# Kernel tuning notes

Hardware: AMD Instinct MI355X
Metric: run time of the kernel (lower is better)

Reference implementation:

```python
import jax, jax.numpy as jnp
import numpy as np
from functools import lru_cache


@lru_cache(maxsize=None)
def _mw_basis(L):
    """Fully-normalized associated Legendre basis on MW-style theta grid.

    Returns (Pfull, w):
      Pfull: (L, 2L-1, L) float32, Pfull[l, L-1+m, t] = Nbar_lm * P_l^m(cos theta_t)
             (zero for |m| > l), with Y_lm = Pfull * exp(i m phi).
      w:     (L,) float32 quadrature weights sin(theta)*dtheta*dphi.
    """
    t = np.arange(L)
    theta = np.pi * (2 * t + 1) / (2 * L - 1)  # MW theta samples
    ct, st = np.cos(theta), np.sin(theta)
    P = np.zeros((L, L, L))
    P[0, 0] = np.full(L, np.sqrt(1.0 / (4.0 * np.pi)))
    for m in range(1, L):
        P[m, m] = -np.sqrt((2.0 * m + 1.0) / (2.0 * m)) * st * P[m - 1, m - 1]
    for m in range(L - 1):
        P[m + 1, m] = np.sqrt(2.0 * m + 3.0) * ct * P[m, m]
    for m in range(L):
        for l in range(m + 2, L):
            a = np.sqrt((4.0 * l * l - 1.0) / (l * l - m * m))
            b = np.sqrt(((2.0 * l + 1.0) * (l - 1 - m) * (l - 1 + m)) / ((2.0 * l - 3.0) * (l * l - m * m)))
            P[l, m] = a * ct * P[l - 1, m] - b * P[l - 2, m]
    Pfull = np.zeros((L, 2 * L - 1, L), dtype=np.float32)
    for m in range(L):
        Pfull[:, L - 1 + m, :] = P[:, m, :]
        if m > 0:
            Pfull[:, L - 1 - m, :] = ((-1.0) ** m) * P[:, m, :]
    dang = 2.0 * np.pi / (2 * L - 1)  # theta and phi spacing
    w = (st * dang * dang).astype(np.float32)
    return jnp.asarray(Pfull), jnp.asarray(w)


def sht_forward(x):
    """x: (L, 2L-1, C) real -> flm: (L, 2L-1, C) complex, m indexed -(L-1)..(L-1)."""
    L = x.shape[0]
    P, w = _mw_basis(L)
    F = jnp.fft.fft(x.astype(jnp.complex64), axis=1)           # k = 0..2L-2
    F = jnp.concatenate([F[:, L:, :], F[:, :L, :]], axis=1)     # reorder to m = -(L-1)..L-1
    # flm = sum_t w_t Nbar P_l^m(theta_t) * Fm(theta_t)
    return jnp.einsum('lmt,tmc->lmc', P * w[None, None, :], F)


def sht_inverse(flm):
    """flm: (L, 2L-1, C) complex -> f: (L, 2L-1, C) complex on MW grid."""
    L = flm.shape[0]
    P, _ = _mw_basis(L)
    G = jnp.einsum('lmc,lmt->tmc', flm, P)                      # (theta, m, C)
    G = jnp.concatenate([G[:, L - 1:, :], G[:, :L - 1, :]], axis=1)  # m order -> fft k order
    return jnp.fft.ifft(G, axis=1) * (2 * L - 1)


def zero_pad_flm(flm, L_out):
    L_in = flm.shape[0]
    p = L_out - L_in
    return jnp.pad(flm, ((0, p), (p, p), (0, 0)))


L_IN = 256
L_FREQ = 128
L_OUT = 256
C_IN = 32
C_OUT = 32
T_DIM = 256


def setup_inputs() -> dict:
    key = jax.random.key(0)
    ks = jax.random.split(key, 8)
    return {
        'x': jax.random.normal(ks[0], (L_IN, 2 * L_IN - 1, C_IN), jnp.float32),
        't_emb': jax.random.normal(ks[1], (T_DIM,), jnp.float32),
        'weight_real': 0.02 * jax.random.normal(ks[2], (L_FREQ, C_IN, C_OUT), jnp.float32),
        'weight_imag': 0.02 * jax.random.normal(ks[3], (L_FREQ, C_IN, C_OUT), jnp.float32),
        'w_tr': jax.random.normal(ks[4], (T_DIM, L_FREQ), jnp.float32) / np.sqrt(T_DIM),
        'b_tr': jnp.zeros((L_FREQ,), jnp.float32),
        'w_ti': jax.random.normal(ks[5], (T_DIM, L_FREQ), jnp.float32) / np.sqrt(T_DIM),
        'b_ti': jnp.zeros((L_FREQ,), jnp.float32),
    }


def reference(x, t_emb, weight_real, weight_imag, w_tr, b_tr, w_ti, b_ti):
    # forward SHT over all channels at once
    flm = sht_forward(x)                                       # (L_in, 2L_in-1, C_in) complex64
    # bilinear resize of the spectrum to the used bandlimit (real/imag separately)
    tgt = (L_FREQ, 2 * L_FREQ - 1, flm.shape[2])
    flm = (jax.image.resize(jnp.real(flm), tgt, 'bilinear')
           + 1j * jax.image.resize(jnp.imag(flm), tgt, 'bilinear'))
    # time-modulated per-degree complex spectral weights
    t_cplx = (t_emb @ w_tr + b_tr) + 1j * (t_emb @ w_ti + b_ti)   # (L_freq,)
    weight = t_cplx[:, None, None] * (weight_real + 1j * weight_imag)  # (L_freq, C_in, C_out)
    flm = jnp.einsum('lmi,lio->lmo', flm, weight)
    # zero pad to output bandlimit and inverse SHT
    flm = zero_pad_flm(flm, L_OUT)                             # (L_out, 2L_out-1, C_out)
    x_out = jnp.real(sht_inverse(flm))
    return x_out
```

## Files before the change

### kernel.cpp

```cpp
#include <hip/hip_runtime.h>
#include <math.h>

#define PI_D 3.14159265358979323846

typedef short v8s __attribute__((ext_vector_type(8)));
typedef float v4f __attribute__((ext_vector_type(4)));

constexpr size_t OFF_PA   = 0;
constexpr size_t OFF_PT   = 8388608;
constexpr size_t OFF_SFRE = 12582912;
constexpr size_t OFF_SFIM = 14680064;
constexpr size_t OFF_FRE  = 16777216;
constexpr size_t OFF_FIM  = 18874368;
constexpr size_t OFF_CRE  = 20971520;
constexpr size_t OFF_CIM  = 22016000;
constexpr size_t OFF_AF   = 23060480;
constexpr size_t OFF_AI   = 23191552;
constexpr size_t OFF_WQ   = 23322624;
constexpr size_t OFF_TC   = 23322880;
constexpr size_t OFF_WLW  = 23323136;
constexpr size_t OFF_WLI  = 23323648;
constexpr size_t OFF_WMW  = 23324160;
constexpr size_t OFF_WMI  = 23325696;
constexpr size_t OFF_GRE  = OFF_FRE;
constexpr size_t OFF_GIM  = OFF_FIM;

__device__ __forceinline__ short f2bf(float f) {
  unsigned u = __float_as_uint(f);
  unsigned r = (u + 0x7FFFu + ((u >> 16) & 1u)) >> 16;
  return (short)r;
}

__global__ void k_prep(const float* t_emb, const float* w_tr, const float* b_tr,
                       const float* w_ti, const float* b_ti, float* ws) {
  int bx = blockIdx.x, tid = threadIdx.x;
  if (bx < 2048) {
    int g = bx * 256 + tid;
    bool inv = (g >= 262144);
    int gid = inv ? g - 262144 : g;
    int j = gid & 7, lane = (gid >> 3) & 63, ks = (gid >> 9) & 15, mt = gid >> 13;
    int m = mt * 16 + (lane & 15);
    int k = ks * 32 + ((lane >> 4) << 3) + j;
    float v = 0.f;
    if (!inv) {
      if (k < 511) {
        int mm = (m < 256) ? m : m - 256;
        int kk = (mm * k) % 511;
        float ang = (float)(2.0 * PI_D / 511.0) * (float)kk;
        float s, c; __sincosf(ang, &s, &c);
        v = (m < 256) ? c : -s;
      }
      ((short*)(ws + OFF_AF))[gid] = f2bf(v);
    } else {
      if (m < 511 && k < 510) {
        int jj = (k < 255) ? k : k - 255;
        int jm = jj - 127;
        int kk = ((jm * m) % 511 + 511) % 511;
        float ang = (float)(2.0 * PI_D / 511.0) * (float)kk;
        float s, c; __sincosf(ang, &s, &c);
        v = (k < 255) ? c : -s;
      }
      ((short*)(ws + OFF_AI))[gid] = f2bf(v);
    }
    return;
  }
  if (tid < 256) {
    double theta = PI_D * (2.0 * tid + 1.0) / 511.0;
    double dang = 2.0 * PI_D / 511.0;
    ws[OFF_WQ + tid] = (float)(sin(theta) * dang * dang);
  }
  {
    int h = tid >> 7, o = tid & 127;
    const float* W = h ? w_ti : w_tr;
    float s = h ? b_ti[o] : b_tr[o];
    for (int T = 0; T < 256; ++T) s += t_emb[T] * W[T * 128 + o];
    ws[OFF_TC + h * 128 + o] = s;
  }
  if (tid < 128) {
    double sf = 2.0 * tid + 0.5;
    double wv[4]; int iv[4]; double wsum = 0.0;
    for (int a = 0; a < 4; ++a) {
      int t = 2 * tid - 1 + a;
      double r = 1.0 - fabs(sf - (double)t) * 0.5;
      bool valid = (t >= 0 && t < 256 && r > 0.0);
      wv[a] = valid ? r : 0.0; iv[a] = valid ? t : 0;
      wsum += wv[a];
    }
    for (int a = 0; a < 4; ++a) {
      ws[OFF_WLW + tid * 4 + a] = (float)(wv[a] / wsum);
      ((int*)(ws + OFF_WLI))[tid * 4 + a] = iv[a];
    }
  }
  if (tid < 255) {
    double inv2 = 511.0 / 255.0;
    double sf = (tid + 0.5) * inv2 - 0.5;
    int t0 = (int)floor(sf) - 2;
    double wv[6]; int iv[6]; double wsum = 0.0;
    for (int b = 0; b < 6; ++b) {
      int t = t0 + b;
      double r = 1.0 - fabs(sf - (double)t) * (255.0 / 511.0);
      bool valid = (t >= 0 && t < 511 && r > 0.0);
      wv[b] = valid ? r : 0.0; iv[b] = valid ? t : 0;
      wsum += wv[b];
    }
    for (int b = 0; b < 6; ++b) {
      ws[OFF_WMW + tid * 6 + b] = (float)(wv[b] / wsum);
      ((int*)(ws + OFF_WMI))[tid * 6 + b] = iv[b];
    }
  }
}

__global__ __launch_bounds__(256) void k_legendre(float* ws) {
  int m = blockIdx.x, t = threadIdx.x;
  __shared__ double cA[256], cB[256], cS[256];
  {
    int l = t;
    if (l >= 1) cS[l] = -sqrt((2.0 * l + 1.0) / (2.0 * l));
    if (l >= m + 2) {
      double ll = l, mm = m;
      double den = ll * ll - mm * mm;
      cA[l] = sqrt((4.0 * ll * ll - 1.0) / den);
      cB[l] = sqrt((2.0 * ll + 1.0) * (ll - 1.0 - mm) * (ll - 1.0 + mm) /
                   ((2.0 * ll - 3.0) * den));
    }
  }
  __syncthreads();
  __shared__ short tile[16 * 280];
  __shared__ short tileT[256 * 34];
  bool wantPT = (m < 128);
  short* PAp = (short*)(ws + OFF_PA) + (size_t)m * 65536;
  short* PTp = (short*)(ws + OFF_PT) + (size_t)m * 65536;
  double theta = PI_D * (2.0 * t + 1.0) / 511.0;
  double ct = cos(theta), st = sin(theta);
  double p0 = sqrt(1.0 / (4.0 * PI_D));
  for (int k = 1; k <= m; ++k) p0 *= cS[k] * st;
  double pm1 = 0.0, pcur = 0.0;
  for (int lt = 0; lt < 16; ++lt) {
    for (int li = 0; li < 16; ++li) {
      int l = lt * 16 + li;
      float v;
      if (l < m) v = 0.f;
      else if (l == m) { pcur = p0; v = (float)pcur; }
      else if (l == m + 1) { pm1 = pcur; pcur = sqrt(2.0 * m + 3.0) * ct * pm1; v = (float)pcur; }
      else { double p2 = cA[l] * ct * pcur - cB[l] * pm1; pm1 = pcur; pcur = p2; v = (float)p2; }
      short bv = f2bf(v);
      tile[li * 280 + t] = bv;
      if (wantPT) tileT[t * 34 + li] = bv;
    }
    __syncthreads();
#pragma unroll
    for (int pass = 0; pass < 2; ++pass) {
      int ch = pass * 256 + t;
      int li = ch & 15, T0 = ch >> 4;
      size_t dst = (size_t)lt * 4096 + (size_t)(T0 >> 2) * 512 + (size_t)((T0 & 3) * 16 + li) * 8;
      *(v8s*)(PAp + dst) = *(const v8s*)(tile + li * 280 + T0 * 8);
    }
    if (wantPT) {
#pragma unroll
      for (int pass = 0; pass < 2; ++pass) {
        int ch = pass * 256 + t;
        int tt = ch >> 1, li0 = (ch & 1) * 8;
        size_t dst = (size_t)(tt >> 4) * 4096 + (size_t)(lt >> 1) * 512 +
                     (size_t)(((lt & 1) * 2 + (li0 >> 3)) * 16 + (tt & 15)) * 8;
        const int* src = (const int*)(tileT + tt * 34 + li0);
        int* d = (int*)(PTp + dst);
        d[0] = src[0]; d[1] = src[1]; d[2] = src[2]; d[3] = src[3];
      }
    }
    __syncthreads();
  }
}

__global__ __launch_bounds__(256) void k_gemm_f(const float* x, float* ws) {
  int bx = blockIdx.x, t = blockIdx.y;
  int nt = bx & 1, mh = bx >> 1;
  int tid = threadIdx.x, wave = tid >> 6, lane = tid & 63;
  const v8s* A = (const v8s*)(ws + OFF_AF);
  float wq = ws[OFF_WQ + t];
  const float* xb = x + (size_t)t * 511 * 32 + nt * 16 + (lane & 15);
  int phiB = (lane >> 4) << 3;
  int mtB = mh * 16 + wave * 4;
  v4f acc[4];
#pragma unroll
  for (int i = 0; i < 4; ++i) acc[i] = (v4f){0.f, 0.f, 0.f, 0.f};
  float bv[8];
#pragma unroll
  for (int j = 0; j < 8; ++j) {
    int phi = phiB + j;
    bv[j] = (phi < 511) ? xb[(size_t)phi * 32] : 0.f;
  }
  for (int ks = 0; ks < 16; ++ks) {
    float bn[8];
    if (ks < 15) {
      int phi0 = (ks + 1) * 32 + phiB;
#pragma unroll
      for (int j = 0; j < 8; ++j) {
        int phi = phi0 + j;
        bn[j] = (phi < 511) ? xb[(size_t)phi * 32] : 0.f;
      }
    }
    v8s b;
#pragma unroll
    for (int j = 0; j < 8; ++j) b[j] = f2bf(wq * bv[j]);
#pragma unroll
    for (int i = 0; i < 4; ++i) {
      v8s a = A[(size_t)((mtB + i) * 16 + ks) * 64 + lane];
      acc[i] = __builtin_amdgcn_mfma_f32_16x16x32_bf16(a, b, acc[i], 0, 0, 0);
    }
    if (ks < 15) {
#pragma unroll
      for (int j = 0; j < 8; ++j) bv[j] = bn[j];
    }
  }
  int quad = lane >> 4, cn = nt * 16 + (lane & 15);
#pragma unroll
  for (int i = 0; i < 4; ++i) {
    int mt = mtB + i;
#pragma unroll
    for (int r = 0; r < 4; ++r) {
      int mp = mt * 16 + quad * 4 + r;
      float v = acc[i][r];
      if (mp < 256) ws[OFF_FRE + ((size_t)mp * 256 + t) * 32 + cn] = v;
      else          ws[OFF_FIM + ((size_t)(mp - 256) * 256 + t) * 32 + cn] = v;
    }
  }
}

__global__ __launch_bounds__(1024) void k_legfwd(float* ws) {
  int m = blockIdx.x;
  int tid = threadIdx.x, mt = tid >> 6, lane = tid & 63;
  const v8s* A = (const v8s*)(ws + OFF_PA) + (size_t)m * 8192;
  int cl = lane & 15, tB = (lane >> 4) << 3;
  int quad = lane >> 4;
  v4f acc[4];
#pragma unroll
  for (int n = 0; n < 4; ++n) acc[n] = (v4f){0.f, 0.f, 0.f, 0.f};
  bool sk = (mt * 16 + 15) < m;
  if (!sk) {
    const float* Fb[4];
#pragma unroll
    for (int n = 0; n < 4; ++n) {
      int cp = n * 16 + cl;
      Fb[n] = ws + (cp < 32 ? OFF_FRE : OFF_FIM) + (size_t)m * 8192 + (size_t)tB * 32 + (cp & 31);
    }
    float bv[4][8];
#pragma unroll
    for (int n = 0; n < 4; ++n)
#pragma unroll
      for (int j = 0; j < 8; ++j) bv[n][j] = Fb[n][(size_t)j * 32];
    for (int ks = 0; ks < 8; ++ks) {
      float bn[4][8];
      if (ks < 7) {
#pragma unroll
        for (int n = 0; n < 4; ++n)
#pragma unroll
          for (int j = 0; j < 8; ++j) bn[n][j] = Fb[n][(size_t)((ks + 1) * 32 + j) * 32];
      }
      v8s a = A[(size_t)mt * 512 + ks * 64 + lane];
#pragma unroll
      for (int n = 0; n < 4; ++n) {
        v8s b;
#pragma unroll
        for (int j = 0; j < 8; ++j) b[j] = f2bf(bv[n][j]);
        acc[n] = __builtin_amdgcn_mfma_f32_16x16x32_bf16(a, b, acc[n], 0, 0, 0);
      }
      if (ks < 7) {
#pragma unroll
        for (int n = 0; n < 4; ++n)
#pragma unroll
          for (int j = 0; j < 8; ++j) bv[n][j] = bn[n][j];
      }
    }
  }
#pragma unroll
  for (int n = 0; n < 4; ++n) {
    int cp = n * 16 + cl;
    float* dst = ws + ((cp >= 32) ? OFF_SFIM : OFF_SFRE) + (size_t)m * 8192 + (cp & 31);
#pragma unroll
    for (int r = 0; r < 4; ++r) {
      int l = mt * 16 + quad * 4 + r;
      dst[(size_t)l * 32] = sk ? 0.f : acc[n][r];
    }
  }
}

__global__ __launch_bounds__(256) void k_conv(const float* w_real, const float* w_imag, float* ws) {
  int jq = blockIdx.x, l = blockIdx.y;
  int tid = threadIdx.x;
  int jl = tid >> 5, o = tid & 31;
  __shared__ __align__(16) float wr[32 * 36];
  __shared__ __align__(16) float wi[32 * 36];
  __shared__ __align__(16) float fr[8 * 32];
  __shared__ __align__(16) float fi[8 * 32];
  {
    int oo = tid >> 3, i4 = (tid & 7) * 4;
    float tcr = ws[OFF_TC + l], tci = ws[OFF_TC + 128 + l];
#pragma unroll
    for (int q = 0; q < 4; ++q) {
      int i = i4 + q;
      float a = w_real[(size_t)l * 1024 + i * 32 + oo];
      float b = w_imag[(size_t)l * 1024 + i * 32 + oo];
      wr[oo * 36 + i] = tcr * a - tci * b;
      wi[oo * 36 + i] = tcr * b + tci * a;
    }
  }
  const float* SFRE = ws + OFF_SFRE;
  const float* SFIM = ws + OFF_SFIM;
  const float* WMW = ws + OFF_WMW;
  const int* WMI = (const int*)(ws + OFF_WMI);
  float wl[4]; int liv[4];
#pragma unroll
  for (int a = 0; a < 4; ++a) {
    wl[a] = ws[OFF_WLW + l * 4 + a];
    liv[a] = ((const int*)(ws + OFF_WLI))[l * 4 + a];
  }
  for (int ji = 0; ji < 8; ++ji) {
    int j = jq * 64 + ji * 8 + jl;
    int jp = (j < 255) ? j : 254;
    float accr = 0.f, acci = 0.f;
    for (int b = 0; b < 6; ++b) {
      float wm = WMW[jp * 6 + b];
      int jm = WMI[jp * 6 + b];
      bool mneg = (jm < 255);
      int mm = mneg ? (255 - jm) : (jm - 255);
      float fre_f = (mneg && (mm & 1)) ? -1.f : 1.f;
      float fim_f = mneg ? -fre_f : 1.f;
#pragma unroll
      for (int a = 0; a < 4; ++a) {
        float w = wm * wl[a];
        size_t base = ((size_t)mm * 256 + liv[a]) * 32 + o;
        accr = fmaf(w * fre_f, SFRE[base], accr);
        acci = fmaf(w * fim_f, SFIM[base], acci);
      }
    }
    __syncthreads();
    fr[jl * 32 + o] = accr;
    fi[jl * 32 + o] = acci;
    __syncthreads();
    float sr = 0.f, si = 0.f;
#pragma unroll
    for (int i0 = 0; i0 < 32; i0 += 4) {
      float4 f_r = *(const float4*)(fr + jl * 32 + i0);
      float4 f_i = *(const float4*)(fi + jl * 32 + i0);
      float4 w_r = *(const float4*)(wr + o * 36 + i0);
      float4 w_i = *(const float4*)(wi + o * 36 + i0);
      sr += f_r.x * w_r.x - f_i.x * w_i.x;  si += f_r.x * w_i.x + f_i.x * w_r.x;
      sr += f_r.y * w_r.y - f_i.y * w_i.y;  si += f_r.y * w_i.y + f_i.y * w_r.y;
      sr += f_r.z * w_r.z - f_i.z * w_i.z;  si += f_r.z * w_i.z + f_i.z * w_r.z;
      sr += f_r.w * w_r.w - f_i.w * w_i.w;  si += f_r.w * w_i.w + f_i.w * w_r.w;
    }
    if (j < 255) {
      float s = (j < 127 && ((127 - j) & 1)) ? -1.f : 1.f;
      ws[OFF_CRE + ((size_t)j * 128 + l) * 32 + o] = s * sr;
      ws[OFF_CIM + ((size_t)j * 128 + l) * 32 + o] = s * si;
    }
  }
}

__global__ __launch_bounds__(1024) void k_gemm_linv(float* ws) {
  int j = blockIdx.x;
  int d = j - 127; int mm = (d < 0) ? -d : d;
  int tid = threadIdx.x, mt = tid >> 6, lane = tid & 63;
  const v8s* A = (const v8s*)(ws + OFF_PT) + (size_t)mm * 8192;
  int cl = lane & 15, lB = (lane >> 4) << 3;
  int quad = lane >> 4;
  v4f acc[4];
#pragma unroll
  for (int n = 0; n < 4; ++n) acc[n] = (v4f){0.f, 0.f, 0.f, 0.f};
  int ks0 = mm >> 5;
  const float* Cb[4];
#pragma unroll
  for (int n = 0; n < 4; ++n) {
    int cp = n * 16 + cl;
    Cb[n] = ws + (cp < 32 ? OFF_CRE : OFF_CIM) + ((size_t)j * 128 + lB) * 32 + (cp & 31);
  }
  float bv[4][8];
#pragma unroll
  for (int n = 0; n < 4; ++n)
#pragma unroll
    for (int j8 = 0; j8 < 8; ++j8) bv[n][j8] = Cb[n][(size_t)(ks0 * 32 + j8) * 32];
  for (int ks = ks0; ks < 4; ++ks) {
    float bn[4][8];
    if (ks < 3) {
#pragma unroll
      for (int n = 0; n < 4; ++n)
#pragma unroll
        for (int j8 = 0; j8 < 8; ++j8) bn[n][j8] = Cb[n][(size_t)((ks + 1) * 32 + j8) * 32];
    }
    v8s a = A[(size_t)mt * 512 + ks * 64 + lane];
#pragma unroll
    for (int n = 0; n < 4; ++n) {
      v8s b;
#pragma unroll
      for (int j8 = 0; j8 < 8; ++j8) b[j8] = f2bf(bv[n][j8]);
      acc[n] = __builtin_amdgcn_mfma_f32_16x16x32_bf16(a, b, acc[n], 0, 0, 0);
    }
    if (ks < 3) {
#pragma unroll
      for (int n = 0; n < 4; ++n)
#pragma unroll
        for (int j8 = 0; j8 < 8; ++j8) bv[n][j8] = bn[n][j8];
    }
  }
#pragma unroll
  for (int n = 0; n < 4; ++n) {
    int cp = n * 16 + cl;
    float* dst = ws + ((cp >= 32) ? OFF_GIM : OFF_GRE) + (size_t)(cp & 31);
#pragma unroll
    for (int r = 0; r < 4; ++r) {
      int t = mt * 16 + quad * 4 + r;
      dst[((size_t)t * 255 + j) * 32] = acc[n][r];
    }
  }
}

__global__ __launch_bounds__(256) void k_gemm_i(const float* ws, float* out) {
  int bx = blockIdx.x, t = blockIdx.y;
  int nt = bx & 1, mh = bx >> 1;
  int tid = threadIdx.x, wave = tid >> 6, lane = tid & 63;
  const v8s* A = (const v8s*)(ws + OFF_AI);
  const float* GRE = ws + OFF_GRE;
  const float* GIM = ws + OFF_GIM;
  int mtB = mh * 16 + wave * 4;
  int cn = nt * 16 + (lane & 15);
  int kB = (lane >> 4) << 3;
  v4f acc[4];
#pragma unroll
  for (int i = 0; i < 4; ++i) acc[i] = (v4f){0.f, 0.f, 0.f, 0.f};
  float bv[8];
#pragma unroll
  for (int j8 = 0; j8 < 8; ++j8) {
    int k = kB + j8;
    float v = 0.f;
    if (k < 255)      v = GRE[((size_t)t * 255 + k) * 32 + cn];
    else if (k < 510) v = GIM[((size_t)t * 255 + (k - 255)) * 32 + cn];
    bv[j8] = v;
  }
  for (int ks = 0; ks < 16; ++ks) {
    float bn[8];
    if (ks < 15) {
      int k0 = (ks + 1) * 32 + kB;
#pragma unroll
      for (int j8 = 0; j8 < 8; ++j8) {
        int k = k0 + j8;
        float v = 0.f;
        if (k < 255)      v = GRE[((size_t)t * 255 + k) * 32 + cn];
        else if (k < 510) v = GIM[((size_t)t * 255 + (k - 255)) * 32 + cn];
        bn[j8] = v;
      }
    }
    v8s b;
#pragma unroll
    for (int j8 = 0; j8 < 8; ++j8) b[j8] = f2bf(bv[j8]);
#pragma unroll
    for (int i = 0; i < 4; ++i) {
      v8s a = A[(size_t)((mtB + i) * 16 + ks) * 64 + lane];
      acc[i] = __builtin_amdgcn_mfma_f32_16x16x32_bf16(a, b, acc[i], 0, 0, 0);
    }
    if (ks < 15) {
#pragma unroll
      for (int j8 = 0; j8 < 8; ++j8) bv[j8] = bn[j8];
    }
  }
  int quad = lane >> 4;
#pragma unroll
  for (int i = 0; i < 4; ++i) {
    int mt = mtB + i;
#pragma unroll
    for (int r = 0; r < 4; ++r) {
      int phi = mt * 16 + quad * 4 + r;
      if (phi < 511) out[((size_t)t * 511 + phi) * 32 + cn] = acc[i][r];
    }
  }
}

extern "C" void kernel_launch(void* const* d_in, const int* in_sizes, int n_in,
                              void* d_out, int out_size, void* d_ws, size_t ws_size,
                              hipStream_t stream) {
  const float* x = (const float*)d_in[0];
  const float* t_emb = (const float*)d_in[1];
  const float* w_real = (const float*)d_in[2];
  const float* w_imag = (const float*)d_in[3];
  const float* w_tr = (const float*)d_in[4];
  const float* b_tr = (const float*)d_in[5];
  const float* w_ti = (const float*)d_in[6];
  const float* b_ti = (const float*)d_in[7];
  float* ws = (float*)d_ws;
  float* out = (float*)d_out;
  (void)in_sizes; (void)n_in; (void)out_size; (void)ws_size;

  hipLaunchKernelGGL(k_prep, dim3(2049), dim3(256), 0, stream,
                     t_emb, w_tr, b_tr, w_ti, b_ti, ws);
  hipLaunchKernelGGL(k_legendre, dim3(256), dim3(256), 0, stream, ws);
  hipLaunchKernelGGL(k_gemm_f, dim3(4, 256), dim3(256), 0, stream, x, ws);
  hipLaunchKernelGGL(k_legfwd, dim3(256), dim3(1024), 0, stream, ws);
  hipLaunchKernelGGL(k_conv, dim3(4, 128), dim3(256), 0, stream, w_real, w_imag, ws);
  hipLaunchKernelGGL(k_gemm_linv, dim3(255), dim3(1024), 0, stream, ws);
  hipLaunchKernelGGL(k_gemm_i, dim3(4, 256), dim3(256), 0, stream, ws, out);
}
```

Measured before the change: 223.2 us.

## Merge prep with Legendre, split big blocks, prefetch MFMA A operands

Merges the prep and Legendre-table kernels into one launch, so the two independent setup phases run concurrently and one launch is saved. Splits the 1024-thread legfwd and linv blocks into four 256-thread blocks and halves the per-block work in conv, giving more, smaller blocks for occupancy and load balance. Software-prefetches the MFMA A fragments one k-step ahead in all GEMM phases to hide load latency. The cost is more registers per thread and shared memory that is statically sized at 32KB.

```diff
diff --git a/kernel.cpp b/kernel.cpp
--- a/kernel.cpp
+++ b/kernel.cpp
@@ -31,11 +31,11 @@
   return (short)r;
 }
 
-__global__ void k_prep(const float* t_emb, const float* w_tr, const float* b_tr,
-                       const float* w_ti, const float* b_ti, float* ws) {
-  int bx = blockIdx.x, tid = threadIdx.x;
-  if (bx < 2048) {
-    int g = bx * 256 + tid;
+
+__device__ void phase_prep(const float* t_emb, const float* w_tr, const float* b_tr,
+                           const float* w_ti, const float* b_ti, float* ws, int g0, int tid) {
+  if (g0 < 2048) {
+    int g = g0 * 256 + tid;
     bool inv = (g >= 262144);
     int gid = inv ? g - 262144 : g;
     int j = gid & 7, lane = (gid >> 3) & 63, ks = (gid >> 9) & 15, mt = gid >> 13;
@@ -110,9 +110,12 @@
   }
 }
 
-__global__ __launch_bounds__(256) void k_legendre(float* ws) {
-  int m = blockIdx.x, t = threadIdx.x;
-  __shared__ double cA[256], cB[256], cS[256];
+__device__ void phase_legendre(float* ws, char* smem, int m, int t) {
+  double* cA = (double*)smem;
+  double* cB = cA + 256;
+  double* cS = cB + 256;
+  short* tile = (short*)(smem + 6144);
+  short* tileT = (short*)(smem + 6144 + 8960);
   {
     int l = t;
     if (l >= 1) cS[l] = -sqrt((2.0 * l + 1.0) / (2.0 * l));
@@ -125,8 +128,6 @@
     }
   }
   __syncthreads();
-  __shared__ short tile[16 * 280];
-  __shared__ short tileT[256 * 34];
   bool wantPT = (m < 128);
   short* PAp = (short*)(ws + OFF_PA) + (size_t)m * 65536;
   short* PTp = (short*)(ws + OFF_PT) + (size_t)m * 65536;
@@ -171,10 +172,9 @@
   }
 }
 
-__global__ __launch_bounds__(256) void k_gemm_f(const float* x, float* ws) {
-  int bx = blockIdx.x, t = blockIdx.y;
-  int nt = bx & 1, mh = bx >> 1;
-  int tid = threadIdx.x, wave = tid >> 6, lane = tid & 63;
+__device__ void phase_gemm_f(const float* x, float* ws, int uid, int tid) {
+  int nt = uid & 1, mh = (uid >> 1) & 1, t = uid >> 2;
+  int wave = tid >> 6, lane = tid & 63;
   const v8s* A = (const v8s*)(ws + OFF_AF);
   float wq = ws[OFF_WQ + t];
   const float* xb = x + (size_t)t * 511 * 32 + nt * 16 + (lane & 15);
@@ -184,11 +184,14 @@
 #pragma unroll
   for (int i = 0; i < 4; ++i) acc[i] = (v4f){0.f, 0.f, 0.f, 0.f};
   float bv[8];
+  v8s a_cur[4], a_nxt[4];
 #pragma unroll
   for (int j = 0; j < 8; ++j) {
     int phi = phiB + j;
     bv[j] = (phi < 511) ? xb[(size_t)phi * 32] : 0.f;
   }
+#pragma unroll
+  for (int i = 0; i < 4; ++i) a_cur[i] = A[(size_t)((mtB + i) * 16 + 0) * 64 + lane];
   for (int ks = 0; ks < 16; ++ks) {
     float bn[8];
     if (ks < 15) {
@@ -198,18 +201,21 @@
         int phi = phi0 + j;
         bn[j] = (phi < 511) ? xb[(size_t)phi * 32] : 0.f;
       }
+#pragma unroll
+      for (int i = 0; i < 4; ++i)
+        a_nxt[i] = A[(size_t)((mtB + i) * 16 + ks + 1) * 64 + lane];
     }
     v8s b;
 #pragma unroll
     for (int j = 0; j < 8; ++j) b[j] = f2bf(wq * bv[j]);
 #pragma unroll
-    for (int i = 0; i < 4; ++i) {
-      v8s a = A[(size_t)((mtB + i) * 16 + ks) * 64 + lane];
-      acc[i] = __builtin_amdgcn_mfma_f32_16x16x32_bf16(a, b, acc[i], 0, 0, 0);
-    }
+    for (int i = 0; i < 4; ++i)
+      acc[i] = __builtin_amdgcn_mfma_f32_16x16x32_bf16(a_cur[i], b, acc[i], 0, 0, 0);
     if (ks < 15) {
 #pragma unroll
       for (int j = 0; j < 8; ++j) bv[j] = bn[j];
+#pragma unroll
+      for (int i = 0; i < 4; ++i) a_cur[i] = a_nxt[i];
     }
   }
   int quad = lane >> 4, cn = nt * 16 + (lane & 15);
@@ -226,9 +232,9 @@
   }
 }
 
-__global__ __launch_bounds__(1024) void k_legfwd(float* ws) {
-  int m = blockIdx.x;
-  int tid = threadIdx.x, mt = tid >> 6, lane = tid & 63;
+__device__ void phase_legfwd(float* ws, int uid, int tid) {
+  int m = uid >> 2;
+  int mt = (uid & 3) * 4 + (tid >> 6), lane = tid & 63;
   const v8s* A = (const v8s*)(ws + OFF_PA) + (size_t)m * 8192;
   int cl = lane & 15, tB = (lane >> 4) << 3;
   int quad = lane >> 4;
@@ -244,31 +250,34 @@
       Fb[n] = ws + (cp < 32 ? OFF_FRE : OFF_FIM) + (size_t)m * 8192 + (size_t)tB * 32 + (cp & 31);
     }
     float bv[4][8];
+    v8s a_cur = A[(size_t)mt * 512 + lane];
 #pragma unroll
     for (int n = 0; n < 4; ++n)
 #pragma unroll
       for (int j = 0; j < 8; ++j) bv[n][j] = Fb[n][(size_t)j * 32];
     for (int ks = 0; ks < 8; ++ks) {
       float bn[4][8];
+      v8s a_nxt;
       if (ks < 7) {
 #pragma unroll
         for (int n = 0; n < 4; ++n)
 #pragma unroll
           for (int j = 0; j < 8; ++j) bn[n][j] = Fb[n][(size_t)((ks + 1) * 32 + j) * 32];
-      }
-      v8s a = A[(size_t)mt * 512 + ks * 64 + lane];
+        a_nxt = A[(size_t)mt * 512 + (ks + 1) * 64 + lane];
+      }
 #pragma unroll
       for (int n = 0; n < 4; ++n) {
         v8s b;
 #pragma unroll
         for (int j = 0; j < 8; ++j) b[j] = f2bf(bv[n][j]);
-        acc[n] = __builtin_amdgcn_mfma_f32_16x16x32_bf16(a, b, acc[n], 0, 0, 0);
+        acc[n] = __builtin_amdgcn_mfma_f32_16x16x32_bf16(a_cur, b, acc[n], 0, 0, 0);
       }
       if (ks < 7) {
 #pragma unroll
         for (int n = 0; n < 4; ++n)
 #pragma unroll
           for (int j = 0; j < 8; ++j) bv[n][j] = bn[n][j];
+        a_cur = a_nxt;
       }
     }
   }
@@ -284,14 +293,14 @@
   }
 }
 
-__global__ __launch_bounds__(256) void k_conv(const float* w_real, const float* w_imag, float* ws) {
-  int jq = blockIdx.x, l = blockIdx.y;
-  int tid = threadIdx.x;
+__device__ void phase_conv(const float* w_real, const float* w_imag, float* ws, char* smem,
+                           int uid, int tid) {
+  int l = uid >> 3, jq8 = uid & 7;
   int jl = tid >> 5, o = tid & 31;
-  __shared__ __align__(16) float wr[32 * 36];
-  __shared__ __align__(16) float wi[32 * 36];
-  __shared__ __align__(16) float fr[8 * 32];
-  __shared__ __align__(16) float fi[8 * 32];
+  float* wr = (float*)smem;
+  float* wi = wr + 32 * 36;
+  float* fr = wi + 32 * 36;
+  float* fi = fr + 8 * 32;
   {
     int oo = tid >> 3, i4 = (tid & 7) * 4;
     float tcr = ws[OFF_TC + l], tci = ws[OFF_TC + 128 + l];
@@ -314,8 +323,8 @@
     wl[a] = ws[OFF_WLW + l * 4 + a];
     liv[a] = ((const int*)(ws + OFF_WLI))[l * 4 + a];
   }
-  for (int ji = 0; ji < 8; ++ji) {
-    int j = jq * 64 + ji * 8 + jl;
+  for (int ji = 0; ji < 4; ++ji) {
+    int j = jq8 * 32 + ji * 8 + jl;
     int jp = (j < 255) ? j : 254;
     float accr = 0.f, acci = 0.f;
     for (int b = 0; b < 6; ++b) {
@@ -357,10 +366,10 @@
   }
 }
 
-__global__ __launch_bounds__(1024) void k_gemm_linv(float* ws) {
-  int j = blockIdx.x;
+__device__ void phase_linv(float* ws, int uid, int tid) {
+  int j = uid >> 2;
   int d = j - 127; int mm = (d < 0) ? -d : d;
-  int tid = threadIdx.x, mt = tid >> 6, lane = tid & 63;
+  int mt = (uid & 3) * 4 + (tid >> 6), lane = tid & 63;
   const v8s* A = (const v8s*)(ws + OFF_PT) + (size_t)mm * 8192;
   int cl = lane & 15, lB = (lane >> 4) << 3;
   int quad = lane >> 4;
@@ -375,31 +384,34 @@
     Cb[n] = ws + (cp < 32 ? OFF_CRE : OFF_CIM) + ((size_t)j * 128 + lB) * 32 + (cp & 31);
   }
   float bv[4][8];
+  v8s a_cur = A[(size_t)mt * 512 + ks0 * 64 + lane];
 #pragma unroll
   for (int n = 0; n < 4; ++n)
 #pragma unroll
     for (int j8 = 0; j8 < 8; ++j8) bv[n][j8] = Cb[n][(size_t)(ks0 * 32 + j8) * 32];
   for (int ks = ks0; ks < 4; ++ks) {
     float bn[4][8];
+    v8s a_nxt;
     if (ks < 3) {
 #pragma unroll
       for (int n = 0; n < 4; ++n)
 #pragma unroll
         for (int j8 = 0; j8 < 8; ++j8) bn[n][j8] = Cb[n][(size_t)((ks + 1) * 32 + j8) * 32];
-    }
-    v8s a = A[(size_t)mt * 512 + ks * 64 + lane];
+      a_nxt = A[(size_t)mt * 512 + (ks + 1) * 64 + lane];
+    }
 #pragma unroll
     for (int n = 0; n < 4; ++n) {
       v8s b;
 #pragma unroll
       for (int j8 = 0; j8 < 8; ++j8) b[j8] = f2bf(bv[n][j8]);
-      acc[n] = __builtin_amdgcn_mfma_f32_16x16x32_bf16(a, b, acc[n], 0, 0, 0);
+      acc[n] = __builtin_amdgcn_mfma_f32_16x16x32_bf16(a_cur, b, acc[n], 0, 0, 0);
     }
     if (ks < 3) {
 #pragma unroll
       for (int n = 0; n < 4; ++n)
 #pragma unroll
         for (int j8 = 0; j8 < 8; ++j8) bv[n][j8] = bn[n][j8];
+      a_cur = a_nxt;
     }
   }
 #pragma unroll
@@ -414,10 +426,9 @@
   }
 }
 
-__global__ __launch_bounds__(256) void k_gemm_i(const float* ws, float* out) {
-  int bx = blockIdx.x, t = blockIdx.y;
-  int nt = bx & 1, mh = bx >> 1;
-  int tid = threadIdx.x, wave = tid >> 6, lane = tid & 63;
+__device__ void phase_gemm_i(const float* ws, float* out, int uid, int tid) {
+  int nt = uid & 1, mh = (uid >> 1) & 1, t = uid >> 2;
+  int wave = tid >> 6, lane = tid & 63;
   const v8s* A = (const v8s*)(ws + OFF_AI);
   const float* GRE = ws + OFF_GRE;
   const float* GIM = ws + OFF_GIM;
@@ -428,6 +439,7 @@
 #pragma unroll
   for (int i = 0; i < 4; ++i) acc[i] = (v4f){0.f, 0.f, 0.f, 0.f};
   float bv[8];
+  v8s a_cur[4], a_nxt[4];
 #pragma unroll
   for (int j8 = 0; j8 < 8; ++j8) {
     int k = kB + j8;
@@ -436,6 +448,8 @@
     else if (k < 510) v = GIM[((size_t)t * 255 + (k - 255)) * 32 + cn];
     bv[j8] = v;
   }
+#pragma unroll
+  for (int i = 0; i < 4; ++i) a_cur[i] = A[(size_t)((mtB + i) * 16 + 0) * 64 + lane];
   for (int ks = 0; ks < 16; ++ks) {
     float bn[8];
     if (ks < 15) {
@@ -448,18 +462,21 @@
         else if (k < 510) v = GIM[((size_t)t * 255 + (k - 255)) * 32 + cn];
         bn[j8] = v;
       }
+#pragma unroll
+      for (int i = 0; i < 4; ++i)
+        a_nxt[i] = A[(size_t)((mtB + i) * 16 + ks + 1) * 64 + lane];
     }
     v8s b;
 #pragma unroll
     for (int j8 = 0; j8 < 8; ++j8) b[j8] = f2bf(bv[j8]);
 #pragma unroll
-    for (int i = 0; i < 4; ++i) {
-      v8s a = A[(size_t)((mtB + i) * 16 + ks) * 64 + lane];
-      acc[i] = __builtin_amdgcn_mfma_f32_16x16x32_bf16(a, b, acc[i], 0, 0, 0);
-    }
+    for (int i = 0; i < 4; ++i)
+      acc[i] = __builtin_amdgcn_mfma_f32_16x16x32_bf16(a_cur[i], b, acc[i], 0, 0, 0);
     if (ks < 15) {
 #pragma unroll
       for (int j8 = 0; j8 < 8; ++j8) bv[j8] = bn[j8];
+#pragma unroll
+      for (int i = 0; i < 4; ++i) a_cur[i] = a_nxt[i];
     }
   }
   int quad = lane >> 4;
@@ -472,6 +489,31 @@
       if (phi < 511) out[((size_t)t * 511 + phi) * 32 + cn] = acc[i][r];
     }
   }
+}
+
+__global__ __launch_bounds__(256) void k_prepleg(const float* t_emb, const float* w_tr,
+                                                 const float* b_tr, const float* w_ti,
+                                                 const float* b_ti, float* ws) {
+  __shared__ __align__(16) char smem[32768];
+  int bid = blockIdx.x;
+  if (bid < 2049) phase_prep(t_emb, w_tr, b_tr, w_ti, b_ti, ws, bid, threadIdx.x);
+  else phase_legendre(ws, smem, bid - 2049, threadIdx.x);
+}
+__global__ __launch_bounds__(256) void kw_gemm_f(const float* x, float* ws) {
+  phase_gemm_f(x, ws, blockIdx.x, threadIdx.x);
+}
+__global__ __launch_bounds__(256) void kw_legfwd(float* ws) {
+  phase_legfwd(ws, blockIdx.x, threadIdx.x);
+}
+__global__ __launch_bounds__(256) void kw_conv(const float* w_real, const float* w_imag, float* ws) {
+  __shared__ __align__(16) char smem[32768];
+  phase_conv(w_real, w_imag, ws, smem, blockIdx.x, threadIdx.x);
+}
+__global__ __launch_bounds__(256) void kw_linv(float* ws) {
+  phase_linv(ws, blockIdx.x, threadIdx.x);
+}
+__global__ __launch_bounds__(256) void kw_gemm_i(const float* ws, float* out) {
+  phase_gemm_i(ws, out, blockIdx.x, threadIdx.x);
 }
 
 extern "C" void kernel_launch(void* const* d_in, const int* in_sizes, int n_in,
@@ -489,12 +531,11 @@
   float* out = (float*)d_out;
   (void)in_sizes; (void)n_in; (void)out_size; (void)ws_size;
 
-  hipLaunchKernelGGL(k_prep, dim3(2049), dim3(256), 0, stream,
+  hipLaunchKernelGGL(k_prepleg, dim3(2305), dim3(256), 0, stream,
                      t_emb, w_tr, b_tr, w_ti, b_ti, ws);
-  hipLaunchKernelGGL(k_legendre, dim3(256), dim3(256), 0, stream, ws);
-  hipLaunchKernelGGL(k_gemm_f, dim3(4, 256), dim3(256), 0, stream, x, ws);
-  hipLaunchKernelGGL(k_legfwd, dim3(256), dim3(1024), 0, stream, ws);
-  hipLaunchKernelGGL(k_conv, dim3(4, 128), dim3(256), 0, stream, w_real, w_imag, ws);
-  hipLaunchKernelGGL(k_gemm_linv, dim3(255), dim3(1024), 0, stream, ws);
-  hipLaunchKernelGGL(k_gemm_i, dim3(4, 256), dim3(256), 0, stream, ws, out);
-}
+  hipLaunchKernelGGL(kw_gemm_f, dim3(1024), dim3(256), 0, stream, x, ws);
+  hipLaunchKernelGGL(kw_legfwd, dim3(1024), dim3(256), 0, stream, ws);
+  hipLaunchKernelGGL(kw_conv, dim3(1024), dim3(256), 0, stream, w_real, w_imag, ws);
+  hipLaunchKernelGGL(kw_linv, dim3(1020), dim3(256), 0, stream, ws);
+  hipLaunchKernelGGL(kw_gemm_i, dim3(1024), dim3(256), 0, stream, ws, out);
+}
```

After: 198.1 us. -11.2%, faster.
